# Kernel tuning notes

Hardware: AMD Instinct MI355X
Metric: run time of the kernel (lower is better)

## Reference

```python
import jax, jax.numpy as jnp
import numpy as np

NEG_INF = -1e30

def _rotate_half(x):
    x1, x2 = jnp.split(x, 2, axis=-1)
    return jnp.concatenate([-x2, x1], axis=-1)

def _apply_rope(x, sin, cos):
    # x: [b, t, h, d]; sin/cos: [t, d]
    s = sin[None, :, None, :]
    c = cos[None, :, None, :]
    return x * c + _rotate_half(x) * s

def setup_inputs() -> dict:
    key = jax.random.key(0)
    ks = jax.random.split(key, 5)
    B, T, D, H = 2, 2048, 2048, 16
    hd = D // H
    x = jax.random.normal(ks[0], (B, T, D), dtype=jnp.float32)
    sin = jax.random.normal(ks[1], (T, hd), dtype=jnp.float32)
    cos = jax.random.normal(ks[2], (T, hd), dtype=jnp.float32)
    W_qkv = jax.random.normal(ks[3], (D, D + 2 * hd), dtype=jnp.float32) * (1.0 / np.sqrt(D))
    W_o = jax.random.normal(ks[4], (D, D), dtype=jnp.float32) * (1.0 / np.sqrt(D))
    return {"x": x, "sin": sin, "cos": cos, "W_qkv": W_qkv, "W_o": W_o}

def reference(x, sin, cos, W_qkv, W_o):
    B, T, D = x.shape
    num_heads = 16
    head_dim = D // num_heads
    scale = head_dim ** (-0.5)

    qkv = x @ W_qkv                              # [B, T, D + 2*hd]
    q, k, v = jnp.split(qkv, [D, D + head_dim], axis=-1)
    # q -> [B, H, T, hd]; k, v single KV head -> [B, 1, T, hd]
    q = q.reshape(B, T, num_heads, head_dim).transpose(0, 2, 1, 3)
    k = k[:, :, None, :].transpose(0, 2, 1, 3)   # [B, 1, T, hd]
    v = v[:, :, None, :].transpose(0, 2, 1, 3)

    # module scales q by head_dim^-0.5 BEFORE rope/attention
    q = q * scale

    # apply_rope_safe: transpose to [B, T, H, hd], apply rope, transpose back
    q = _apply_rope(q.transpose(0, 2, 1, 3), sin, cos).transpose(0, 2, 1, 3)
    k = _apply_rope(k.transpose(0, 2, 1, 3), sin, cos).transpose(0, 2, 1, 3)

    k0 = k[:, 0]                                 # [B, T, hd] (MQA shared KV)
    v0 = v[:, 0]

    # jax.nn.dot_product_attention applies its own 1/sqrt(hd) scaling on top
    scores = jnp.einsum('bhqd,bkd->bhqk', q, k0) * scale
    causal = jnp.tril(jnp.ones((T, T), dtype=bool))
    scores = jnp.where(causal[None, None], scores, NEG_INF)
    probs = jax.nn.softmax(scores, axis=-1)
    out = jnp.einsum('bhqk,bkd->bhqd', probs, v0)  # [B, H, T, hd]

    out = out.transpose(0, 2, 1, 3).reshape(B, T, D)
    return out @ W_o
```

## Files before the change

kernel.cpp:

```cpp
#include <hip/hip_runtime.h>
#include <stdint.h>

typedef __bf16 bf16x8_t __attribute__((ext_vector_type(8)));
typedef float f32x4_t __attribute__((ext_vector_type(4)));

#define AS1 __attribute__((address_space(1)))
#define AS3 __attribute__((address_space(3)))

static __device__ __forceinline__ unsigned short f2bf(float f) {
  union { float f; unsigned u; } a;
  a.f = f;
  unsigned r = a.u + 0x7fffu + ((a.u >> 16) & 1u);
  return (unsigned short)(r >> 16);
}

static __device__ __forceinline__ unsigned pack2bf(float lo, float hi) {
  return (unsigned)f2bf(lo) | ((unsigned)f2bf(hi) << 16);
}

__global__ void cvt_bf16_kernel(const float* __restrict__ in, unsigned short* __restrict__ out) {
  long i = ((long)blockIdx.x * blockDim.x + threadIdx.x) * 4;
  float4 v = *(const float4*)(in + i);
  ushort4 o;
  o.x = f2bf(v.x);
  o.y = f2bf(v.y);
  o.z = f2bf(v.z);
  o.w = f2bf(v.w);
  *(ushort4*)(out + i) = o;
}

__global__ void transpose_f32_bf16(const float* __restrict__ src, unsigned short* __restrict__ dst,
                                   int ld, int dld, long sbs, long dbs) {
  __shared__ float tile[64][65];
  src += (long)blockIdx.z * sbs;
  dst += (long)blockIdx.z * dbs;
  const int c0 = blockIdx.x * 64, r0 = blockIdx.y * 64;
  const int tx = threadIdx.x, ty = threadIdx.y;
#pragma unroll
  for (int j = 0; j < 64; j += 4)
    tile[ty + j][tx] = src[(long)(r0 + ty + j) * ld + (c0 + tx)];
  __syncthreads();
#pragma unroll
  for (int j = 0; j < 64; j += 4)
    dst[(long)(c0 + ty + j) * dld + (r0 + tx)] = f2bf(tile[tx][ty + j]);
}

__global__ __launch_bounds__(256) void gemm_bt(const unsigned short* __restrict__ A,
                                               const unsigned short* __restrict__ Bt,
                                               float* __restrict__ C,
                                               int M, int N, int K, int nx) {
  __shared__ unsigned short As[3][128 * 32];
  __shared__ unsigned short Bs[3][128 * 32];
  const int nwg = gridDim.x;
  const int bid = blockIdx.x;
  const int swz = (bid & 7) * (nwg >> 3) + (bid >> 3);
  const int by = swz / nx;
  const int bx = swz - by * nx;

  const int tid = threadIdx.x;
  const int wid = tid >> 6, lane = tid & 63;
  const int r16 = lane & 15, g = lane >> 4;
  const long bm = (long)by * 128;
  const long bn = (long)bx * 128;
  const int wr = (wid >> 1) * 64, wc = (wid & 1) * 64;
  const int gr = g ^ (r16 & 3);
  const int sslot = (lane & 3) ^ ((lane >> 2) & 3);

  f32x4_t acc[4][4];
#pragma unroll
  for (int i = 0; i < 4; i++)
#pragma unroll
    for (int j = 0; j < 4; j++) acc[i][j] = (f32x4_t){0.f, 0.f, 0.f, 0.f};

  const int NT = K >> 5;

#define STAGE_G(buf, kt)                                                              \
  {                                                                                   \
    _Pragma("unroll") for (int i = 0; i < 2; i++) {                                   \
      const int chunk = (i * 4 + wid) * 64 + lane;                                    \
      const int row = chunk >> 2;                                                     \
      __builtin_amdgcn_global_load_lds(                                               \
          (const AS1 void*)(A + (bm + row) * K + (kt) + sslot * 8),                   \
          (AS3 void*)(&As[buf][chunk * 8]), 16, 0, 0);                                \
      __builtin_amdgcn_global_load_lds(                                               \
          (const AS1 void*)(Bt + (bn + row) * K + (kt) + sslot * 8),                  \
          (AS3 void*)(&Bs[buf][chunk * 8]), 16, 0, 0);                                \
    }                                                                                 \
  }

  STAGE_G(0, 0)
  STAGE_G(1, 32)
  asm volatile("s_waitcnt vmcnt(4)" ::: "memory");
  __builtin_amdgcn_s_barrier();

  for (int T = 0; T < NT; T++) {
    const int cur = T % 3;
    if (T + 2 < NT) {
      const int nb = (T + 2) % 3;
      STAGE_G(nb, (T + 2) * 32)
    }
    __builtin_amdgcn_sched_barrier(0);
    bf16x8_t af[4], bfr[4];
#pragma unroll
    for (int mi = 0; mi < 4; mi++)
      af[mi] = *(const bf16x8_t*)(&As[cur][(wr + mi * 16 + r16) * 32 + gr * 8]);
#pragma unroll
    for (int ni = 0; ni < 4; ni++)
      bfr[ni] = *(const bf16x8_t*)(&Bs[cur][(wc + ni * 16 + r16) * 32 + gr * 8]);
    __builtin_amdgcn_s_setprio(1);
#pragma unroll
    for (int mi = 0; mi < 4; mi++)
#pragma unroll
      for (int ni = 0; ni < 4; ni++)
        acc[mi][ni] = __builtin_amdgcn_mfma_f32_16x16x32_bf16(af[mi], bfr[ni], acc[mi][ni], 0, 0, 0);
    __builtin_amdgcn_s_setprio(0);
    if (T + 2 < NT)
      asm volatile("s_waitcnt vmcnt(4)" ::: "memory");
    else
      asm volatile("s_waitcnt vmcnt(0)" ::: "memory");
    __builtin_amdgcn_s_barrier();
  }
#undef STAGE_G

#pragma unroll
  for (int mi = 0; mi < 4; mi++)
#pragma unroll
    for (int ni = 0; ni < 4; ni++) {
      const long rowb = bm + wr + mi * 16 + 4 * g;
      const long colb = bn + wc + ni * 16 + r16;
#pragma unroll
      for (int j = 0; j < 4; j++)
        C[(rowb + j) * N + colb] = acc[mi][ni][j];
    }
}

__global__ void rope_kernel(const float* __restrict__ qkv,
                            const float* __restrict__ sinp,
                            const float* __restrict__ cosp,
                            unsigned short* __restrict__ qr,
                            unsigned short* __restrict__ kr) {
  const int row = blockIdx.x;
  const int b = row >> 11, t = row & 2047;
  const float* src = qkv + (long)row * 2304;
  const int tid = threadIdx.x;
  const int d = tid & 127;
  const int dp = (d + 64) & 127;
  const float c = cosp[t * 128 + d];
  const float s = sinp[t * 128 + d];
  const float sgn = (d < 64) ? -1.f : 1.f;
  for (int h = (tid >> 7); h < 16; h += 2) {
    const float x0 = src[h * 128 + d];
    const float xp = src[h * 128 + dp];
    qr[((long)((b * 16 + h) * 2048 + t)) * 128 + d] = f2bf((x0 * c + sgn * xp * s) * 0.0078125f);
  }
  if (tid < 128) {
    const float x0 = src[2048 + d];
    const float xp = src[2048 + dp];
    kr[((long)(b * 2048 + t)) * 128 + d] = f2bf(x0 * c + sgn * xp * s);
  }
}

__global__ __launch_bounds__(256, 2)
void mqa_attn(const unsigned short* __restrict__ qr,
              const unsigned short* __restrict__ kr,
              const unsigned short* __restrict__ vT,
              unsigned short* __restrict__ ao) {
  __shared__ unsigned short Kb[2][64 * 128];
  __shared__ unsigned short Vb[128 * 64];
  __shared__ unsigned short plds[4][16 * 64];
  const int idx = blockIdx.x;
  const int pj = idx & 15, h = (idx >> 4) & 15, b = idx >> 8;
  const int tid = threadIdx.x;
  const int wid = tid >> 6, lane = tid & 63;
  const int r = lane & 15, g = lane >> 4;
  const int rs = r & 7;
  char* pw = (char*)&plds[wid][0];

  const unsigned short* kbase = kr + (long)b * 2048 * 128;
  const unsigned short* vbase = vT + (long)b * 128 * 2048;
  const unsigned short* qh = qr + (long)(b * 16 + h) * 2048 * 128;

  const int scol = (tid & 15) ^ ((tid >> 4) & 7);
  const int vscol = (tid & 7) ^ ((tid >> 3) & 7);

  f32x4_t o[8];
#pragma unroll
  for (int i = 0; i < 8; i++) o[i] = (f32x4_t){0.f, 0.f, 0.f, 0.f};
  float m = 0.f, lsum = 0.f;

  int tile = pj;
  bf16x8_t qf[4];
  {
    const unsigned short* qp = qh + (long)(tile * 64 + wid * 16 + r) * 128 + g * 8;
#pragma unroll
    for (int c = 0; c < 4; c++) qf[c] = *(const bf16x8_t*)(qp + c * 32);
  }

#pragma unroll
  for (int i = 0; i < 4; i++) {
    const int row = i * 16 + (tid >> 4);
    __builtin_amdgcn_global_load_lds(
        (const AS1 void*)(kbase + (long)row * 128 + scol * 8),
        (AS3 void*)(&Kb[0][(i * 256 + tid) * 8]), 16, 0, 0);
  }
  asm volatile("s_waitcnt vmcnt(0)" ::: "memory");
  __builtin_amdgcn_s_barrier();

  const int switch_s = pj + 1;
  for (int s = 0; s <= 32; s++) {
    const int cur = s & 1;
    const int kv0 = (s <= pj) ? 64 * s : 64 * (s - 1 - pj);

    if (s == switch_s) {
      float lt = lsum;
      lt += __shfl_xor(lt, 16);
      lt += __shfl_xor(lt, 32);
      float rl[4];
#pragma unroll
      for (int jj = 0; jj < 4; jj++) rl[jj] = 1.0f / __shfl(lt, 4 * g + jj);
      unsigned short* aop = ao + ((long)(b * 2048 + tile * 64 + wid * 16 + 4 * g)) * 2048 + h * 128 + r;
#pragma unroll
      for (int dt = 0; dt < 8; dt++)
#pragma unroll
        for (int jj = 0; jj < 4; jj++)
          aop[(long)jj * 2048 + dt * 16] = f2bf(o[dt][jj] * rl[jj]);
      tile = 31 - pj;
      const unsigned short* qp = qh + (long)(tile * 64 + wid * 16 + r) * 128 + g * 8;
#pragma unroll
      for (int c = 0; c < 4; c++) qf[c] = *(const bf16x8_t*)(qp + c * 32);
#pragma unroll
      for (int i = 0; i < 8; i++) o[i] = (f32x4_t){0.f, 0.f, 0.f, 0.f};
      m = 0.f;
      lsum = 0.f;
    }

#pragma unroll
    for (int i = 0; i < 4; i++) {
      const int vrow = i * 32 + (tid >> 3);
      __builtin_amdgcn_global_load_lds(
          (const AS1 void*)(vbase + (long)vrow * 2048 + kv0 + vscol * 8),
          (AS3 void*)(&Vb[(i * 256 + tid) * 8]), 16, 0, 0);
    }
    if (s < 32) {
      const int kvn = (s + 1 <= pj) ? 64 * (s + 1) : 64 * (s - pj);
#pragma unroll
      for (int i = 0; i < 4; i++) {
        const int row = i * 16 + (tid >> 4);
        __builtin_amdgcn_global_load_lds(
            (const AS1 void*)(kbase + (long)(kvn + row) * 128 + scol * 8),
            (AS3 void*)(&Kb[cur ^ 1][(i * 256 + tid) * 8]), 16, 0, 0);
      }
    }
    __builtin_amdgcn_sched_barrier(0);

    f32x4_t sc[4];
#pragma unroll
    for (int t = 0; t < 4; t++) sc[t] = (f32x4_t){0.f, 0.f, 0.f, 0.f};
    const unsigned short* Kcur = &Kb[cur][0];
    __builtin_amdgcn_s_setprio(1);
#pragma unroll
    for (int t = 0; t < 4; t++) {
      const unsigned short* krow = Kcur + (16 * t + r) * 128;
#pragma unroll
      for (int c = 0; c < 4; c++) {
        const bf16x8_t kf = *(const bf16x8_t*)(krow + (((4 * c + g) ^ rs) << 3));
        sc[t] = __builtin_amdgcn_mfma_f32_16x16x32_bf16(kf, qf[c], sc[t], 0, 0, 0);
      }
    }
    __builtin_amdgcn_s_setprio(0);

    if (s == pj || s == 32) {
#pragma unroll
      for (int t = 0; t < 4; t++)
#pragma unroll
        for (int jj = 0; jj < 4; jj++)
          if (t * 16 + 4 * g + jj > wid * 16 + r) sc[t][jj] = -1e30f;
    }
    float lm = sc[0][0];
#pragma unroll
    for (int t = 0; t < 4; t++)
#pragma unroll
      for (int jj = 0; jj < 4; jj++) lm = fmaxf(lm, sc[t][jj]);
    if (!__all(lm <= m + 8.f)) {
      float pm = lm;
      pm = fmaxf(pm, __shfl_xor(pm, 16));
      pm = fmaxf(pm, __shfl_xor(pm, 32));
      const float mnew = fmaxf(m, pm);
      const float alpha = __expf(m - mnew);
      lsum *= alpha;
      float aj[4];
#pragma unroll
      for (int jj = 0; jj < 4; jj++) aj[jj] = __shfl(alpha, 4 * g + jj);
#pragma unroll
      for (int dt = 0; dt < 8; dt++) {
        o[dt][0] *= aj[0]; o[dt][1] *= aj[1]; o[dt][2] *= aj[2]; o[dt][3] *= aj[3];
      }
      m = mnew;
    }
    float p[16];
#pragma unroll
    for (int t = 0; t < 4; t++)
#pragma unroll
      for (int jj = 0; jj < 4; jj++) p[4 * t + jj] = __expf(sc[t][jj] - m);
    float ls = 0.f;
#pragma unroll
    for (int i = 0; i < 16; i++) ls += p[i];
    lsum += ls;

    asm volatile("" ::: "memory");
#pragma unroll
    for (int t = 0; t < 4; t++) {
      uint2 w = {pack2bf(p[4 * t], p[4 * t + 1]), pack2bf(p[4 * t + 2], p[4 * t + 3])};
      *(uint2*)(pw + r * 128 + (((2 * t + (g >> 1)) ^ rs) << 4) + ((g & 1) << 3)) = w;
    }
    asm volatile("s_waitcnt lgkmcnt(0)" ::: "memory");
    const bf16x8_t pa0 = *(const bf16x8_t*)(pw + r * 128 + ((g ^ rs) << 4));
    const bf16x8_t pa1 = *(const bf16x8_t*)(pw + r * 128 + (((4 + g) ^ rs) << 4));

    if (s < 32)
      asm volatile("s_waitcnt vmcnt(4)" ::: "memory");
    else
      asm volatile("s_waitcnt vmcnt(0)" ::: "memory");
    __builtin_amdgcn_s_barrier();

    __builtin_amdgcn_s_setprio(1);
#pragma unroll
    for (int dt = 0; dt < 8; dt++) {
      const bf16x8_t vfA = *(const bf16x8_t*)(Vb + (dt * 16 + r) * 64 + ((g ^ rs) << 3));
      o[dt] = __builtin_amdgcn_mfma_f32_16x16x32_bf16(pa0, vfA, o[dt], 0, 0, 0);
    }
#pragma unroll
    for (int dt = 0; dt < 8; dt++) {
      const bf16x8_t vfB = *(const bf16x8_t*)(Vb + (dt * 16 + r) * 64 + (((4 + g) ^ rs) << 3));
      o[dt] = __builtin_amdgcn_mfma_f32_16x16x32_bf16(pa1, vfB, o[dt], 0, 0, 0);
    }
    __builtin_amdgcn_s_setprio(0);

    asm volatile("s_waitcnt vmcnt(0)" ::: "memory");
    __builtin_amdgcn_s_barrier();
  }
  {
    float lt = lsum;
    lt += __shfl_xor(lt, 16);
    lt += __shfl_xor(lt, 32);
    float rl[4];
#pragma unroll
    for (int jj = 0; jj < 4; jj++) rl[jj] = 1.0f / __shfl(lt, 4 * g + jj);
    unsigned short* aop = ao + ((long)(b * 2048 + tile * 64 + wid * 16 + 4 * g)) * 2048 + h * 128 + r;
#pragma unroll
    for (int dt = 0; dt < 8; dt++)
#pragma unroll
      for (int jj = 0; jj < 4; jj++)
        aop[(long)jj * 2048 + dt * 16] = f2bf(o[dt][jj] * rl[jj]);
  }
}

extern "C" void kernel_launch(void* const* d_in, const int* in_sizes, int n_in,
                              void* d_out, int out_size, void* d_ws, size_t ws_size,
                              hipStream_t stream) {
  const float* x    = (const float*)d_in[0];
  const float* sinp = (const float*)d_in[1];
  const float* cosp = (const float*)d_in[2];
  const float* Wqkv = (const float*)d_in[3];
  const float* Wo   = (const float*)d_in[4];
  float* out = (float*)d_out;
  char* ws = (char*)d_ws;

  const int B = 2, T = 2048, D = 2048, H = 16, HD = 128;
  const int M = B * T;
  const int NQ = D + 2 * HD;

  unsigned short* xb    = (unsigned short*)(ws + 0);
  unsigned short* wqkvT = (unsigned short*)(ws + 16777216);
  unsigned short* woT   = (unsigned short*)(ws + 26214400);
  float*          qkv   = (float*)         (ws + 34603008);
  unsigned short* qr    = (unsigned short*)(ws + 72351744);
  unsigned short* kr    = (unsigned short*)(ws + 89128960);
  unsigned short* vT    = (unsigned short*)(ws + 90177536);
  unsigned short* ao    = xb;

  dim3 tb(64, 4);
  cvt_bf16_kernel<<<(M * D) / 1024, 256, 0, stream>>>(x, xb);
  transpose_f32_bf16<<<dim3(NQ / 64, D / 64, 1), tb, 0, stream>>>(Wqkv, wqkvT, NQ, D, 0, 0);
  transpose_f32_bf16<<<dim3(D / 64, D / 64, 1), tb, 0, stream>>>(Wo, woT, D, D, 0, 0);
  gemm_bt<<<dim3((NQ / 128) * (M / 128)), 256, 0, stream>>>(xb, wqkvT, qkv, M, NQ, D, NQ / 128);
  rope_kernel<<<M, 256, 0, stream>>>(qkv, sinp, cosp, qr, kr);
  transpose_f32_bf16<<<dim3(HD / 64, T / 64, B), tb, 0, stream>>>(
      qkv + 2176, vT, NQ, T, (long)T * NQ, (long)HD * T);
  mqa_attn<<<dim3(512), 256, 0, stream>>>(qr, kr, vT, ao);
  gemm_bt<<<dim3((D / 128) * (M / 128)), 256, 0, stream>>>(ao, woT, out, M, D, D, D / 128);
}
```

Before: 203.0 us.

## Process 128-query tiles per block with two query groups per wave

Each wave now handles 32 query rows (two 16-row groups) against each K/V tile, so every K/V LDS load feeds twice as many MFMAs. The earlier pairing of a light and a heavy causal tile inside one block is dropped. Blocks now each take one 128-row tile, and the launch index order interleaves tiles so heavy and light blocks mix across the grid. Register pressure roughly doubles for accumulators, and load balance now relies on block scheduling rather than tile pairing.

Result: slower. 224.3 us (+10.5%).

```diff
diff --git a/kernel.cpp b/kernel.cpp
--- a/kernel.cpp
+++ b/kernel.cpp
@@ -167,9 +167,11 @@
               unsigned short* __restrict__ ao) {
   __shared__ unsigned short Kb[2][64 * 128];
   __shared__ unsigned short Vb[128 * 64];
-  __shared__ unsigned short plds[4][16 * 64];
+  __shared__ unsigned short plds[4][32 * 64];
   const int idx = blockIdx.x;
-  const int pj = idx & 15, h = (idx >> 4) & 15, b = idx >> 8;
+  const int bh = idx & 31, h = bh & 15, b = bh >> 4;
+  const int chunk = idx >> 5;
+  const int tile = 2 * (chunk & 7) + (chunk >> 3);
   const int tid = threadIdx.x;
   const int wid = tid >> 6, lane = tid & 63;
   const int r = lane & 15, g = lane >> 4;
@@ -183,17 +185,19 @@
   const int scol = (tid & 15) ^ ((tid >> 4) & 7);
   const int vscol = (tid & 7) ^ ((tid >> 3) & 7);
 
-  f32x4_t o[8];
-#pragma unroll
-  for (int i = 0; i < 8; i++) o[i] = (f32x4_t){0.f, 0.f, 0.f, 0.f};
-  float m = 0.f, lsum = 0.f;
-
-  int tile = pj;
-  bf16x8_t qf[4];
-  {
-    const unsigned short* qp = qh + (long)(tile * 64 + wid * 16 + r) * 128 + g * 8;
-#pragma unroll
-    for (int c = 0; c < 4; c++) qf[c] = *(const bf16x8_t*)(qp + c * 32);
+  f32x4_t o[2][8];
+#pragma unroll
+  for (int qg = 0; qg < 2; qg++)
+#pragma unroll
+    for (int i = 0; i < 8; i++) o[qg][i] = (f32x4_t){0.f, 0.f, 0.f, 0.f};
+  float m0 = 0.f, m1 = 0.f, ls0 = 0.f, ls1 = 0.f;
+
+  bf16x8_t qf[2][4];
+#pragma unroll
+  for (int qg = 0; qg < 2; qg++) {
+    const unsigned short* qp = qh + (long)(tile * 128 + wid * 32 + qg * 16 + r) * 128 + g * 8;
+#pragma unroll
+    for (int c = 0; c < 4; c++) qf[qg][c] = *(const bf16x8_t*)(qp + c * 32);
   }
 
 #pragma unroll
@@ -206,33 +210,10 @@
   asm volatile("s_waitcnt vmcnt(0)" ::: "memory");
   __builtin_amdgcn_s_barrier();
 
-  const int switch_s = pj + 1;
-  for (int s = 0; s <= 32; s++) {
+  const int nstg = 2 * tile + 2;
+  for (int s = 0; s < nstg; s++) {
     const int cur = s & 1;
-    const int kv0 = (s <= pj) ? 64 * s : 64 * (s - 1 - pj);
-
-    if (s == switch_s) {
-      float lt = lsum;
-      lt += __shfl_xor(lt, 16);
-      lt += __shfl_xor(lt, 32);
-      float rl[4];
-#pragma unroll
-      for (int jj = 0; jj < 4; jj++) rl[jj] = 1.0f / __shfl(lt, 4 * g + jj);
-      unsigned short* aop = ao + ((long)(b * 2048 + tile * 64 + wid * 16 + 4 * g)) * 2048 + h * 128 + r;
-#pragma unroll
-      for (int dt = 0; dt < 8; dt++)
-#pragma unroll
-        for (int jj = 0; jj < 4; jj++)
-          aop[(long)jj * 2048 + dt * 16] = f2bf(o[dt][jj] * rl[jj]);
-      tile = 31 - pj;
-      const unsigned short* qp = qh + (long)(tile * 64 + wid * 16 + r) * 128 + g * 8;
-#pragma unroll
-      for (int c = 0; c < 4; c++) qf[c] = *(const bf16x8_t*)(qp + c * 32);
-#pragma unroll
-      for (int i = 0; i < 8; i++) o[i] = (f32x4_t){0.f, 0.f, 0.f, 0.f};
-      m = 0.f;
-      lsum = 0.f;
-    }
+    const int kv0 = 64 * s;
 
 #pragma unroll
     for (int i = 0; i < 4; i++) {
@@ -241,8 +222,8 @@
           (const AS1 void*)(vbase + (long)vrow * 2048 + kv0 + vscol * 8),
           (AS3 void*)(&Vb[(i * 256 + tid) * 8]), 16, 0, 0);
     }
-    if (s < 32) {
-      const int kvn = (s + 1 <= pj) ? 64 * (s + 1) : 64 * (s - pj);
+    if (s + 1 < nstg) {
+      const int kvn = 64 * (s + 1);
 #pragma unroll
       for (int i = 0; i < 4; i++) {
         const int row = i * 16 + (tid >> 4);
@@ -253,9 +234,11 @@
     }
     __builtin_amdgcn_sched_barrier(0);
 
-    f32x4_t sc[4];
-#pragma unroll
-    for (int t = 0; t < 4; t++) sc[t] = (f32x4_t){0.f, 0.f, 0.f, 0.f};
+    f32x4_t sc[2][4];
+#pragma unroll
+    for (int qg = 0; qg < 2; qg++)
+#pragma unroll
+      for (int t = 0; t < 4; t++) sc[qg][t] = (f32x4_t){0.f, 0.f, 0.f, 0.f};
     const unsigned short* Kcur = &Kb[cur][0];
     __builtin_amdgcn_s_setprio(1);
 #pragma unroll
@@ -264,60 +247,89 @@
 #pragma unroll
       for (int c = 0; c < 4; c++) {
         const bf16x8_t kf = *(const bf16x8_t*)(krow + (((4 * c + g) ^ rs) << 3));
-        sc[t] = __builtin_amdgcn_mfma_f32_16x16x32_bf16(kf, qf[c], sc[t], 0, 0, 0);
+        sc[0][t] = __builtin_amdgcn_mfma_f32_16x16x32_bf16(kf, qf[0][c], sc[0][t], 0, 0, 0);
+        sc[1][t] = __builtin_amdgcn_mfma_f32_16x16x32_bf16(kf, qf[1][c], sc[1][t], 0, 0, 0);
       }
     }
     __builtin_amdgcn_s_setprio(0);
 
-    if (s == pj || s == 32) {
-#pragma unroll
-      for (int t = 0; t < 4; t++)
-#pragma unroll
-        for (int jj = 0; jj < 4; jj++)
-          if (t * 16 + 4 * g + jj > wid * 16 + r) sc[t][jj] = -1e30f;
-    }
-    float lm = sc[0][0];
+    if (s >= 2 * tile) {
+      const int sub = s - 2 * tile;
+#pragma unroll
+      for (int qg = 0; qg < 2; qg++)
+#pragma unroll
+        for (int t = 0; t < 4; t++)
+#pragma unroll
+          for (int jj = 0; jj < 4; jj++)
+            if (64 * sub + 16 * t + 4 * g + jj > wid * 32 + qg * 16 + r) sc[qg][t][jj] = -1e30f;
+    }
+    float lm0 = sc[0][0][0], lm1 = sc[1][0][0];
 #pragma unroll
     for (int t = 0; t < 4; t++)
 #pragma unroll
-      for (int jj = 0; jj < 4; jj++) lm = fmaxf(lm, sc[t][jj]);
-    if (!__all(lm <= m + 8.f)) {
-      float pm = lm;
-      pm = fmaxf(pm, __shfl_xor(pm, 16));
-      pm = fmaxf(pm, __shfl_xor(pm, 32));
-      const float mnew = fmaxf(m, pm);
-      const float alpha = __expf(m - mnew);
-      lsum *= alpha;
-      float aj[4];
-#pragma unroll
-      for (int jj = 0; jj < 4; jj++) aj[jj] = __shfl(alpha, 4 * g + jj);
-#pragma unroll
-      for (int dt = 0; dt < 8; dt++) {
-        o[dt][0] *= aj[0]; o[dt][1] *= aj[1]; o[dt][2] *= aj[2]; o[dt][3] *= aj[3];
+      for (int jj = 0; jj < 4; jj++) {
+        lm0 = fmaxf(lm0, sc[0][t][jj]);
+        lm1 = fmaxf(lm1, sc[1][t][jj]);
       }
-      m = mnew;
-    }
-    float p[16];
+    if (!__all(lm0 <= m0 + 8.f && lm1 <= m1 + 8.f)) {
+      float pm0 = lm0, pm1 = lm1;
+      pm0 = fmaxf(pm0, __shfl_xor(pm0, 16));
+      pm0 = fmaxf(pm0, __shfl_xor(pm0, 32));
+      pm1 = fmaxf(pm1, __shfl_xor(pm1, 16));
+      pm1 = fmaxf(pm1, __shfl_xor(pm1, 32));
+      const float mn0 = fmaxf(m0, pm0), mn1 = fmaxf(m1, pm1);
+      const float a0 = __expf(m0 - mn0), a1 = __expf(m1 - mn1);
+      ls0 *= a0;
+      ls1 *= a1;
+      float aj0[4], aj1[4];
+#pragma unroll
+      for (int jj = 0; jj < 4; jj++) {
+        aj0[jj] = __shfl(a0, 4 * g + jj);
+        aj1[jj] = __shfl(a1, 4 * g + jj);
+      }
+#pragma unroll
+      for (int dt = 0; dt < 8; dt++)
+#pragma unroll
+        for (int jj = 0; jj < 4; jj++) {
+          o[0][dt][jj] *= aj0[jj];
+          o[1][dt][jj] *= aj1[jj];
+        }
+      m0 = mn0;
+      m1 = mn1;
+    }
+    float p0[16], p1[16];
 #pragma unroll
     for (int t = 0; t < 4; t++)
 #pragma unroll
-      for (int jj = 0; jj < 4; jj++) p[4 * t + jj] = __expf(sc[t][jj] - m);
-    float ls = 0.f;
-#pragma unroll
-    for (int i = 0; i < 16; i++) ls += p[i];
-    lsum += ls;
+      for (int jj = 0; jj < 4; jj++) {
+        p0[4 * t + jj] = __expf(sc[0][t][jj] - m0);
+        p1[4 * t + jj] = __expf(sc[1][t][jj] - m1);
+      }
+    float a0 = 0.f, a1 = 0.f;
+#pragma unroll
+    for (int i = 0; i < 16; i++) {
+      a0 += p0[i];
+      a1 += p1[i];
+    }
+    ls0 += a0;
+    ls1 += a1;
 
     asm volatile("" ::: "memory");
 #pragma unroll
     for (int t = 0; t < 4; t++) {
-      uint2 w = {pack2bf(p[4 * t], p[4 * t + 1]), pack2bf(p[4 * t + 2], p[4 * t + 3])};
-      *(uint2*)(pw + r * 128 + (((2 * t + (g >> 1)) ^ rs) << 4) + ((g & 1) << 3)) = w;
+      uint2 w0 = {pack2bf(p0[4 * t], p0[4 * t + 1]), pack2bf(p0[4 * t + 2], p0[4 * t + 3])};
+      uint2 w1 = {pack2bf(p1[4 * t], p1[4 * t + 1]), pack2bf(p1[4 * t + 2], p1[4 * t + 3])};
+      const int slot = (((2 * t + (g >> 1)) ^ rs) << 4) + ((g & 1) << 3);
+      *(uint2*)(pw + r * 128 + slot) = w0;
+      *(uint2*)(pw + (16 + r) * 128 + slot) = w1;
     }
     asm volatile("s_waitcnt lgkmcnt(0)" ::: "memory");
-    const bf16x8_t pa0 = *(const bf16x8_t*)(pw + r * 128 + ((g ^ rs) << 4));
-    const bf16x8_t pa1 = *(const bf16x8_t*)(pw + r * 128 + (((4 + g) ^ rs) << 4));
-
-    if (s < 32)
+    const bf16x8_t pa00 = *(const bf16x8_t*)(pw + r * 128 + ((g ^ rs) << 4));
+    const bf16x8_t pa01 = *(const bf16x8_t*)(pw + r * 128 + (((4 + g) ^ rs) << 4));
+    const bf16x8_t pa10 = *(const bf16x8_t*)(pw + (16 + r) * 128 + ((g ^ rs) << 4));
+    const bf16x8_t pa11 = *(const bf16x8_t*)(pw + (16 + r) * 128 + (((4 + g) ^ rs) << 4));
+
+    if (s + 1 < nstg)
       asm volatile("s_waitcnt vmcnt(4)" ::: "memory");
     else
       asm volatile("s_waitcnt vmcnt(0)" ::: "memory");
@@ -327,31 +339,35 @@
 #pragma unroll
     for (int dt = 0; dt < 8; dt++) {
       const bf16x8_t vfA = *(const bf16x8_t*)(Vb + (dt * 16 + r) * 64 + ((g ^ rs) << 3));
-      o[dt] = __builtin_amdgcn_mfma_f32_16x16x32_bf16(pa0, vfA, o[dt], 0, 0, 0);
+      o[0][dt] = __builtin_amdgcn_mfma_f32_16x16x32_bf16(pa00, vfA, o[0][dt], 0, 0, 0);
+      o[1][dt] = __builtin_amdgcn_mfma_f32_16x16x32_bf16(pa10, vfA, o[1][dt], 0, 0, 0);
     }
 #pragma unroll
     for (int dt = 0; dt < 8; dt++) {
       const bf16x8_t vfB = *(const bf16x8_t*)(Vb + (dt * 16 + r) * 64 + (((4 + g) ^ rs) << 3));
-      o[dt] = __builtin_amdgcn_mfma_f32_16x16x32_bf16(pa1, vfB, o[dt], 0, 0, 0);
+      o[0][dt] = __builtin_amdgcn_mfma_f32_16x16x32_bf16(pa01, vfB, o[0][dt], 0, 0, 0);
+      o[1][dt] = __builtin_amdgcn_mfma_f32_16x16x32_bf16(pa11, vfB, o[1][dt], 0, 0, 0);
     }
     __builtin_amdgcn_s_setprio(0);
 
     asm volatile("s_waitcnt vmcnt(0)" ::: "memory");
     __builtin_amdgcn_s_barrier();
   }
-  {
-    float lt = lsum;
+#pragma unroll
+  for (int qg = 0; qg < 2; qg++) {
+    float lt = (qg == 0) ? ls0 : ls1;
     lt += __shfl_xor(lt, 16);
     lt += __shfl_xor(lt, 32);
     float rl[4];
 #pragma unroll
     for (int jj = 0; jj < 4; jj++) rl[jj] = 1.0f / __shfl(lt, 4 * g + jj);
-    unsigned short* aop = ao + ((long)(b * 2048 + tile * 64 + wid * 16 + 4 * g)) * 2048 + h * 128 + r;
+    unsigned short* aop =
+        ao + ((long)(b * 2048 + tile * 128 + wid * 32 + qg * 16 + 4 * g)) * 2048 + h * 128 + r;
 #pragma unroll
     for (int dt = 0; dt < 8; dt++)
 #pragma unroll
       for (int jj = 0; jj < 4; jj++)
-        aop[(long)jj * 2048 + dt * 16] = f2bf(o[dt][jj] * rl[jj]);
+        aop[(long)jj * 2048 + dt * 16] = f2bf(o[qg][dt][jj] * rl[jj]);
   }
 }
 
```

## Double-buffer V tiles, use exp2 with folded log2e, hardware bf16 pack

Applied to the files above, without the earlier changes.

V is now double-buffered in LDS and prefetched one iteration ahead together with the next K tile. The waitcnt and barrier sequence is reworked so the global-to-LDS loads overlap the QK and PV MFMA work instead of stalling on the current V tile. The softmax switches to exp2, with log2(e) folded into the q scaling in the rope kernel and the rescale threshold adjusted to match. The software bf16 rounding used when packing probabilities is replaced by the v_cvt_pk_bf16_f32 instruction. The second V buffer doubles V's LDS footprint, which may pressure the two-blocks-per-CU occupancy target.

Result: no change. 202.8 us, median of 2 (-0.1%).

```diff
diff --git a/kernel.cpp b/kernel.cpp
--- a/kernel.cpp
+++ b/kernel.cpp
@@ -14,8 +14,10 @@
   return (unsigned short)(r >> 16);
 }
 
-static __device__ __forceinline__ unsigned pack2bf(float lo, float hi) {
-  return (unsigned)f2bf(lo) | ((unsigned)f2bf(hi) << 16);
+static __device__ __forceinline__ unsigned cvtpk(float lo, float hi) {
+  unsigned r;
+  asm("v_cvt_pk_bf16_f32 %0, %1, %2" : "=v"(r) : "v"(lo), "v"(hi));
+  return r;
 }
 
 __global__ void cvt_bf16_kernel(const float* __restrict__ in, unsigned short* __restrict__ out) {
@@ -151,7 +153,8 @@
   for (int h = (tid >> 7); h < 16; h += 2) {
     const float x0 = src[h * 128 + d];
     const float xp = src[h * 128 + dp];
-    qr[((long)((b * 16 + h) * 2048 + t)) * 128 + d] = f2bf((x0 * c + sgn * xp * s) * 0.0078125f);
+    qr[((long)((b * 16 + h) * 2048 + t)) * 128 + d] =
+        f2bf((x0 * c + sgn * xp * s) * 0.011271055f);
   }
   if (tid < 128) {
     const float x0 = src[2048 + d];
@@ -166,7 +169,7 @@
               const unsigned short* __restrict__ vT,
               unsigned short* __restrict__ ao) {
   __shared__ unsigned short Kb[2][64 * 128];
-  __shared__ unsigned short Vb[128 * 64];
+  __shared__ unsigned short Vb[2][128 * 64];
   __shared__ unsigned short plds[4][16 * 64];
   const int idx = blockIdx.x;
   const int pj = idx & 15, h = (idx >> 4) & 15, b = idx >> 8;
@@ -203,13 +206,19 @@
         (const AS1 void*)(kbase + (long)row * 128 + scol * 8),
         (AS3 void*)(&Kb[0][(i * 256 + tid) * 8]), 16, 0, 0);
   }
+#pragma unroll
+  for (int i = 0; i < 4; i++) {
+    const int vrow = i * 32 + (tid >> 3);
+    __builtin_amdgcn_global_load_lds(
+        (const AS1 void*)(vbase + (long)vrow * 2048 + vscol * 8),
+        (AS3 void*)(&Vb[0][(i * 256 + tid) * 8]), 16, 0, 0);
+  }
   asm volatile("s_waitcnt vmcnt(0)" ::: "memory");
   __builtin_amdgcn_s_barrier();
 
   const int switch_s = pj + 1;
   for (int s = 0; s <= 32; s++) {
     const int cur = s & 1;
-    const int kv0 = (s <= pj) ? 64 * s : 64 * (s - 1 - pj);
 
     if (s == switch_s) {
       float lt = lsum;
@@ -234,13 +243,6 @@
       lsum = 0.f;
     }
 
-#pragma unroll
-    for (int i = 0; i < 4; i++) {
-      const int vrow = i * 32 + (tid >> 3);
-      __builtin_amdgcn_global_load_lds(
-          (const AS1 void*)(vbase + (long)vrow * 2048 + kv0 + vscol * 8),
-          (AS3 void*)(&Vb[(i * 256 + tid) * 8]), 16, 0, 0);
-    }
     if (s < 32) {
       const int kvn = (s + 1 <= pj) ? 64 * (s + 1) : 64 * (s - pj);
 #pragma unroll
@@ -250,6 +252,14 @@
             (const AS1 void*)(kbase + (long)(kvn + row) * 128 + scol * 8),
             (AS3 void*)(&Kb[cur ^ 1][(i * 256 + tid) * 8]), 16, 0, 0);
       }
+      __builtin_amdgcn_sched_barrier(0);
+#pragma unroll
+      for (int i = 0; i < 4; i++) {
+        const int vrow = i * 32 + (tid >> 3);
+        __builtin_amdgcn_global_load_lds(
+            (const AS1 void*)(vbase + (long)vrow * 2048 + kvn + vscol * 8),
+            (AS3 void*)(&Vb[cur ^ 1][(i * 256 + tid) * 8]), 16, 0, 0);
+      }
     }
     __builtin_amdgcn_sched_barrier(0);
 
@@ -276,17 +286,17 @@
         for (int jj = 0; jj < 4; jj++)
           if (t * 16 + 4 * g + jj > wid * 16 + r) sc[t][jj] = -1e30f;
     }
-    float lm = sc[0][0];
-#pragma unroll
-    for (int t = 0; t < 4; t++)
-#pragma unroll
-      for (int jj = 0; jj < 4; jj++) lm = fmaxf(lm, sc[t][jj]);
-    if (!__all(lm <= m + 8.f)) {
+    float mx01 = fmaxf(fmaxf(sc[0][0], sc[0][1]), fmaxf(sc[0][2], sc[0][3]));
+    float mx23 = fmaxf(fmaxf(sc[1][0], sc[1][1]), fmaxf(sc[1][2], sc[1][3]));
+    float mx45 = fmaxf(fmaxf(sc[2][0], sc[2][1]), fmaxf(sc[2][2], sc[2][3]));
+    float mx67 = fmaxf(fmaxf(sc[3][0], sc[3][1]), fmaxf(sc[3][2], sc[3][3]));
+    const float lm = fmaxf(fmaxf(mx01, mx23), fmaxf(mx45, mx67));
+    if (!__all(lm <= m + 11.5f)) {
       float pm = lm;
       pm = fmaxf(pm, __shfl_xor(pm, 16));
       pm = fmaxf(pm, __shfl_xor(pm, 32));
       const float mnew = fmaxf(m, pm);
-      const float alpha = __expf(m - mnew);
+      const float alpha = __builtin_amdgcn_exp2f(m - mnew);
       lsum *= alpha;
       float aj[4];
 #pragma unroll
@@ -301,7 +311,7 @@
 #pragma unroll
     for (int t = 0; t < 4; t++)
 #pragma unroll
-      for (int jj = 0; jj < 4; jj++) p[4 * t + jj] = __expf(sc[t][jj] - m);
+      for (int jj = 0; jj < 4; jj++) p[4 * t + jj] = __builtin_amdgcn_exp2f(sc[t][jj] - m);
     float ls = 0.f;
 #pragma unroll
     for (int i = 0; i < 16; i++) ls += p[i];
@@ -310,33 +320,37 @@
     asm volatile("" ::: "memory");
 #pragma unroll
     for (int t = 0; t < 4; t++) {
-      uint2 w = {pack2bf(p[4 * t], p[4 * t + 1]), pack2bf(p[4 * t + 2], p[4 * t + 3])};
+      uint2 w = {cvtpk(p[4 * t], p[4 * t + 1]), cvtpk(p[4 * t + 2], p[4 * t + 3])};
       *(uint2*)(pw + r * 128 + (((2 * t + (g >> 1)) ^ rs) << 4) + ((g & 1) << 3)) = w;
     }
     asm volatile("s_waitcnt lgkmcnt(0)" ::: "memory");
     const bf16x8_t pa0 = *(const bf16x8_t*)(pw + r * 128 + ((g ^ rs) << 4));
     const bf16x8_t pa1 = *(const bf16x8_t*)(pw + r * 128 + (((4 + g) ^ rs) << 4));
+
+    if (s < 32)
+      asm volatile("s_waitcnt vmcnt(8)" ::: "memory");
+    else
+      asm volatile("s_waitcnt vmcnt(0)" ::: "memory");
+    __builtin_amdgcn_s_barrier();
+
+    const unsigned short* Vcur = &Vb[cur][0];
+    __builtin_amdgcn_s_setprio(1);
+#pragma unroll
+    for (int dt = 0; dt < 8; dt++) {
+      const bf16x8_t vfA = *(const bf16x8_t*)(Vcur + (dt * 16 + r) * 64 + ((g ^ rs) << 3));
+      o[dt] = __builtin_amdgcn_mfma_f32_16x16x32_bf16(pa0, vfA, o[dt], 0, 0, 0);
+    }
+#pragma unroll
+    for (int dt = 0; dt < 8; dt++) {
+      const bf16x8_t vfB = *(const bf16x8_t*)(Vcur + (dt * 16 + r) * 64 + (((4 + g) ^ rs) << 3));
+      o[dt] = __builtin_amdgcn_mfma_f32_16x16x32_bf16(pa1, vfB, o[dt], 0, 0, 0);
+    }
+    __builtin_amdgcn_s_setprio(0);
 
     if (s < 32)
       asm volatile("s_waitcnt vmcnt(4)" ::: "memory");
     else
       asm volatile("s_waitcnt vmcnt(0)" ::: "memory");
-    __builtin_amdgcn_s_barrier();
-
-    __builtin_amdgcn_s_setprio(1);
-#pragma unroll
-    for (int dt = 0; dt < 8; dt++) {
-      const bf16x8_t vfA = *(const bf16x8_t*)(Vb + (dt * 16 + r) * 64 + ((g ^ rs) << 3));
-      o[dt] = __builtin_amdgcn_mfma_f32_16x16x32_bf16(pa0, vfA, o[dt], 0, 0, 0);
-    }
-#pragma unroll
-    for (int dt = 0; dt < 8; dt++) {
-      const bf16x8_t vfB = *(const bf16x8_t*)(Vb + (dt * 16 + r) * 64 + (((4 + g) ^ rs) << 3));
-      o[dt] = __builtin_amdgcn_mfma_f32_16x16x32_bf16(pa1, vfB, o[dt], 0, 0, 0);
-    }
-    __builtin_amdgcn_s_setprio(0);
-
-    asm volatile("s_waitcnt vmcnt(0)" ::: "memory");
     __builtin_amdgcn_s_barrier();
   }
   {
```
